# Kernel optimization log

Measured on AMD Instinct MI355X. Metric: run time of the kernel, lower is better.

The kernel has to match this reference:

```python
import jax, jax.numpy as jnp
import numpy as np

IN_CH = 64
INTER = IN_CH // 2
B, H, W = 2, 80, 80


def setup_inputs() -> dict:
    key = jax.random.key(0)
    k = jax.random.split(key, 5)
    s = 1.0 / np.sqrt(IN_CH)
    return {
        "x": jax.random.normal(k[0], (B, IN_CH, H, W), dtype=jnp.float32),
        "g_w": jax.random.normal(k[1], (INTER, IN_CH), dtype=jnp.float32) * s,
        "theta_w": jax.random.normal(k[2], (INTER, IN_CH), dtype=jnp.float32) * s,
        "phi_w": jax.random.normal(k[3], (INTER, IN_CH), dtype=jnp.float32) * s,
        "w_w": jax.random.normal(k[4], (IN_CH, INTER), dtype=jnp.float32) * (1.0 / np.sqrt(INTER)),
    }


def reference(x, g_w, theta_w, phi_w, w_w):
    # Non-local block: 1x1 convs (bias=False) are channel matmuls over N=H*W positions.
    Bc, C, Hh, Ww = x.shape
    N = Hh * Ww
    xf = x.reshape(Bc, C, N)                            # [B, C, N]
    g = jnp.einsum('ic,bcn->bni', g_w, xf)              # [B, N, inter]
    theta = jnp.einsum('ic,bcn->bni', theta_w, xf)      # [B, N, inter]
    phi = jnp.einsum('ic,bcn->bin', phi_w, xf)          # [B, inter, N]
    affinity = jax.nn.softmax(jnp.einsum('bni,bim->bnm', theta, phi), axis=-1)  # [B, N, N]
    y = jnp.einsum('bnm,bmi->bni', affinity, g)         # [B, N, inter]
    y = jnp.einsum('ci,bni->bcn', w_w, y).reshape(Bc, C, Hh, Ww)
    return x + y
```

## Files before the change

### kernel.cpp

```cpp
#include <hip/hip_runtime.h>
#include <math.h>

#define BATCH 2
#define CH    64
#define INTER 32
#define NPOS  6400
#define NTILE 50
#define LOG2E 1.44269504088896f
#define SPLIT 10
#define TPB   5

typedef _Float16 f16x8 __attribute__((ext_vector_type(8)));
typedef _Float16 f16x2 __attribute__((ext_vector_type(2)));
typedef _Float16 h4    __attribute__((ext_vector_type(4)));
typedef float    f32x4 __attribute__((ext_vector_type(4)));

static __device__ __forceinline__ f16x2 pkrtz(float a, float b) {
    return __builtin_bit_cast(f16x2, __builtin_amdgcn_cvt_pkrtz(a, b));
}


__global__ __launch_bounds__(256) void nlb_proj_kernel(
    const float* __restrict__ x,
    const float* __restrict__ g_w,
    const float* __restrict__ th_w,
    const float* __restrict__ ph_w,
    _Float16* __restrict__ Qh, _Float16* __restrict__ Kf,
    _Float16* __restrict__ Vf)
{
    const int b  = blockIdx.z;
    const int p  = blockIdx.y;
    const int n0 = blockIdx.x * 64;
    const int t  = threadIdx.x;
    const int w  = __builtin_amdgcn_readfirstlane(t) >> 6;
    const int lane = t & 63;

    const float* wsrc = (p == 0) ? th_w : (p == 1) ? ph_w : g_w;
    const float* xg = x + (size_t)b * CH * NPOS + n0 + lane;

    float xr[64];
    #pragma unroll
    for (int c = 0; c < 64; c++) xr[c] = xg[(size_t)c * NPOS];

    __shared__ float buf[32][65];

    float accs[8];
    #pragma unroll
    for (int rr = 0; rr < 8; rr++) {
        const int row = w * 8 + rr;
        const float* wr = wsrc + row * 64;
        float a0 = 0.f, a1 = 0.f, a2 = 0.f, a3 = 0.f;
        #pragma unroll
        for (int c = 0; c < 16; c++) {
            a0 += wr[c]      * xr[c];
            a1 += wr[c + 16] * xr[c + 16];
            a2 += wr[c + 32] * xr[c + 32];
            a3 += wr[c + 48] * xr[c + 48];
        }
        accs[rr] = (a0 + a1) + (a2 + a3);
    }

    if (p == 2) {
        const int n  = n0 + lane;
        const int T  = n >> 7, kk = n & 127;
        const int g  = kk >> 4, qd = (kk >> 2) & 3, r3 = kk & 3;
        const int kc = g >> 1, j = (g & 1) * 4 + r3;
        const int half = w >> 1, d15base = (w & 1) * 8;
        _Float16* vb = Vf +
            (((((size_t)b * NTILE + T) * 8 + kc * 2 + half) * 64
              + qd * 16 + d15base) * 8 + j);
        #pragma unroll
        for (int rr = 0; rr < 8; rr++)
            vb[(size_t)rr * 8] = (_Float16)accs[rr];
        return;
    }

    #pragma unroll
    for (int rr = 0; rr < 8; rr++) buf[w * 8 + rr][lane] = accs[rr];
    __syncthreads();

    const int pos = t >> 2, ic = t & 3;
    if (p == 0) {
        f16x8 hv;
        #pragma unroll
        for (int j = 0; j < 8; j++)
            hv[j] = (_Float16)(buf[ic * 8 + j][pos] * LOG2E);
        *(f16x8*)(Qh + ((size_t)b * NPOS + n0 + pos) * 32 + ic * 8) = hv;
    } else {
        f16x8 hv;
        #pragma unroll
        for (int j = 0; j < 8; j++)
            hv[j] = (_Float16)buf[ic * 8 + j][pos];
        const int key = n0 + pos, T = key >> 7, kk = key & 127;
        const int g = kk >> 4, m16 = kk & 15;
        ((f16x8*)Kf)[(((size_t)b * NTILE + T) * 8 + g) * 64 + ic * 16 + m16] = hv;
    }
}

__global__ __launch_bounds__(512) void nlb_flash_kernel(
    const _Float16* __restrict__ Qh, const _Float16* __restrict__ Kf,
    const _Float16* __restrict__ Vf,
    _Float16* __restrict__ Opart, float2* __restrict__ ml)
{
    __shared__ f16x8 smem[5120];

    const int b     = blockIdx.z;
    const int split = blockIdx.y;
    const int t     = threadIdx.x;
    const int w     = t >> 6;
    const int lane  = t & 63;
    const int n16   = lane & 15;
    const int quad  = lane >> 4;
    const int q0    = blockIdx.x * 128 + w * 16;

    const f16x8 qa = *(const f16x8*)(Qh + ((size_t)b * NPOS + q0 + n16) * 32 + quad * 8);

    {
        const f16x8* Ks = (const f16x8*)Kf + ((size_t)b * NTILE + split * TPB) * 512;
        const f16x8* Vs = (const f16x8*)Vf + ((size_t)b * NTILE + split * TPB) * 512;
        f16x8 st[5];
        #pragma unroll
        for (int c = 0; c < 5; c++) st[c] = Ks[c * 512 + t];
        #pragma unroll
        for (int c = 0; c < 5; c++) smem[c * 512 + t] = st[c];
        #pragma unroll
        for (int c = 0; c < 5; c++) st[c] = Vs[c * 512 + t];
        #pragma unroll
        for (int c = 0; c < 5; c++) smem[2560 + c * 512 + t] = st[c];
    }
    __syncthreads();

    f32x4 o0 = (f32x4)0.f;
    f32x4 o1 = (f32x4)0.f;
    float runm = -1e30f, lsum = 0.f;

    for (int i = 0; i < TPB; i++) {
        const int kb = i * 512;
        const int vb = 2560 + i * 512;

        f32x4 sc[8];
        #pragma unroll
        for (int g = 0; g < 8; g++) {
            f16x8 kf = smem[kb + g * 64 + lane];
            f32x4 z = (f32x4)0.f;
            sc[g] = __builtin_amdgcn_mfma_f32_16x16x32_f16(kf, qa, z, 0, 0, 0);
        }

        float m = fmaxf(fmaxf(sc[0][0], sc[0][1]), fmaxf(sc[0][2], sc[0][3]));
        #pragma unroll
        for (int g = 1; g < 8; g++) {
            float mg = fmaxf(fmaxf(sc[g][0], sc[g][1]), fmaxf(sc[g][2], sc[g][3]));
            m = fmaxf(m, mg);
        }
        m = fmaxf(m, __shfl_xor(m, 16));
        m = fmaxf(m, __shfl_xor(m, 32));
        float nm = fmaxf(runm, m);
        float a  = __builtin_amdgcn_exp2f(runm - nm);
        runm = nm;
        float ls = 0.f;
        #pragma unroll
        for (int g = 0; g < 8; g++) {
            #pragma unroll
            for (int r = 0; r < 4; r++) {
                float p = __builtin_amdgcn_exp2f(sc[g][r] - nm);
                sc[g][r] = p;
                ls += p;
            }
        }
        lsum = lsum * a + ls;
        o0 *= a;
        o1 *= a;

        #pragma unroll
        for (int kc = 0; kc < 4; kc++) {
            union { f16x8 v; f16x2 h2[4]; } pb;
            pb.h2[0] = pkrtz(sc[kc * 2][0],     sc[kc * 2][1]);
            pb.h2[1] = pkrtz(sc[kc * 2][2],     sc[kc * 2][3]);
            pb.h2[2] = pkrtz(sc[kc * 2 + 1][0], sc[kc * 2 + 1][1]);
            pb.h2[3] = pkrtz(sc[kc * 2 + 1][2], sc[kc * 2 + 1][3]);
            f16x8 v0 = smem[vb + (kc * 2) * 64 + lane];
            f16x8 v1 = smem[vb + (kc * 2 + 1) * 64 + lane];
            o0 = __builtin_amdgcn_mfma_f32_16x16x32_f16(v0, pb.v, o0, 0, 0, 0);
            o1 = __builtin_amdgcn_mfma_f32_16x16x32_f16(v1, pb.v, o1, 0, 0, 0);
        }
    }

    lsum += __shfl_xor(lsum, 16);
    lsum += __shfl_xor(lsum, 32);
    float invl = 1.f / lsum;
    const size_t base = ((size_t)(b * SPLIT + split) * NPOS + q0 + n16) * 32;
    h4 h0, h1;
    #pragma unroll
    for (int r = 0; r < 4; r++) {
        h0[r] = (_Float16)(o0[r] * invl);
        h1[r] = (_Float16)(o1[r] * invl);
    }
    *(h4*)(Opart + base + quad * 4)      = h0;
    *(h4*)(Opart + base + 16 + quad * 4) = h1;
    if (quad == 0)
        ml[(size_t)(b * SPLIT + split) * NPOS + q0 + n16] = make_float2(runm, lsum);
}

__global__ __launch_bounds__(256) void nlb_combine_kernel(
    const _Float16* __restrict__ Opart, const float2* __restrict__ ml,
    const float* __restrict__ w_w, const float* __restrict__ x,
    float* __restrict__ out)
{
    __shared__ float wf[64][33];
    __shared__ float wts[32][12];
    __shared__ float of[32][33];

    const int b  = blockIdx.y;
    const int q0 = blockIdx.x * 32;
    const int t  = threadIdx.x;

    for (int idx = t; idx < 2048; idx += 256) wf[idx >> 5][idx & 31] = w_w[idx];

    if (t < 32) {
        float2 v[SPLIT];
        float m = -1e30f;
        #pragma unroll
        for (int s = 0; s < SPLIT; s++) {
            v[s] = ml[(size_t)(b * SPLIT + s) * NPOS + q0 + t];
            m = fmaxf(m, v[s].x);
        }
        float suml = 0.f;
        #pragma unroll
        for (int s = 0; s < SPLIT; s++) {
            float wgt = __builtin_amdgcn_exp2f(v[s].x - m) * v[s].y;
            wts[t][s] = wgt;
            suml += wgt;
        }
        float inv = 1.f / suml;
        #pragma unroll
        for (int s = 0; s < SPLIT; s++) wts[t][s] *= inv;
    }
    __syncthreads();

    {
        const int q = t >> 3, dg = t & 7;
        float a0 = 0.f, a1 = 0.f, a2 = 0.f, a3 = 0.f;
        #pragma unroll
        for (int s = 0; s < SPLIT; s++) {
            h4 hv = *(const h4*)(Opart +
                ((size_t)(b * SPLIT + s) * NPOS + q0 + q) * 32 + dg * 4);
            float c = wts[q][s];
            a0 += c * (float)hv[0]; a1 += c * (float)hv[1];
            a2 += c * (float)hv[2]; a3 += c * (float)hv[3];
        }
        of[q][dg * 4]     = a0; of[q][dg * 4 + 1] = a1;
        of[q][dg * 4 + 2] = a2; of[q][dg * 4 + 3] = a3;
    }
    __syncthreads();

    {
        const int q = t & 31, cg = t >> 5;
        const float* xb = x   + (size_t)b * CH * NPOS + q0 + q;
        float*       ob = out + (size_t)b * CH * NPOS + q0 + q;
        #pragma unroll
        for (int cc = 0; cc < 8; cc++) {
            int ch = cg * 8 + cc;
            float acc = 0.f;
            #pragma unroll
            for (int i = 0; i < 32; i++) acc += wf[ch][i] * of[q][i];
            ob[(size_t)ch * NPOS] = acc + xb[(size_t)ch * NPOS];
        }
    }
}

extern "C" void kernel_launch(void* const* d_in, const int* in_sizes, int n_in,
                              void* d_out, int out_size, void* d_ws, size_t ws_size,
                              hipStream_t stream) {
    const float* x    = (const float*)d_in[0];
    const float* g_w  = (const float*)d_in[1];
    const float* th_w = (const float*)d_in[2];
    const float* ph_w = (const float*)d_in[3];
    const float* w_w  = (const float*)d_in[4];
    float* out = (float*)d_out;

    const size_t SZ = (size_t)BATCH * NPOS * INTER;
    _Float16* Qh = (_Float16*)d_ws;
    _Float16* Kf = Qh + SZ;
    _Float16* Vf = Kf + SZ;
    _Float16* Opart = Vf + SZ;
    float2*   ml    = (float2*)(Opart + SZ * SPLIT);

    nlb_proj_kernel<<<dim3(NPOS / 64, 3, BATCH), 256, 0, stream>>>(
        x, g_w, th_w, ph_w, Qh, Kf, Vf);
    nlb_flash_kernel<<<dim3(NPOS / 128, SPLIT, BATCH), 512, 0, stream>>>(
        Qh, Kf, Vf, Opart, ml);
    nlb_combine_kernel<<<dim3(NPOS / 32, BATCH), 256, 0, stream>>>(
        Opart, ml, w_w, x, out);
}
```

Before: 102.5 us.

## Compute all three projections per block and prefetch V fragments in flash loop

The projection kernel now computes the g, theta and phi projections in one block, so each block loads its 64 channels of x into registers once instead of three separate blocks each loading them. The grid shrinks to one third and extra syncthreads guard reuse of the shared buffer. The flash kernel adds a launch-bounds occupancy hint and loads all eight V fragments from LDS before the softmax, so LDS latency can overlap with the exp and max work. The cost is higher register pressure and fewer, longer-running projection blocks.

```diff
diff --git a/kernel.cpp b/kernel.cpp
--- a/kernel.cpp
+++ b/kernel.cpp
@@ -28,14 +28,12 @@
     _Float16* __restrict__ Qh, _Float16* __restrict__ Kf,
     _Float16* __restrict__ Vf)
 {
-    const int b  = blockIdx.z;
-    const int p  = blockIdx.y;
+    const int b  = blockIdx.y;
     const int n0 = blockIdx.x * 64;
     const int t  = threadIdx.x;
     const int w  = __builtin_amdgcn_readfirstlane(t) >> 6;
     const int lane = t & 63;
 
-    const float* wsrc = (p == 0) ? th_w : (p == 1) ? ph_w : g_w;
     const float* xg = x + (size_t)b * CH * NPOS + n0 + lane;
 
     float xr[64];
@@ -43,24 +41,26 @@
     for (int c = 0; c < 64; c++) xr[c] = xg[(size_t)c * NPOS];
 
     __shared__ float buf[32][65];
-
     float accs[8];
-    #pragma unroll
-    for (int rr = 0; rr < 8; rr++) {
-        const int row = w * 8 + rr;
-        const float* wr = wsrc + row * 64;
-        float a0 = 0.f, a1 = 0.f, a2 = 0.f, a3 = 0.f;
-        #pragma unroll
-        for (int c = 0; c < 16; c++) {
-            a0 += wr[c]      * xr[c];
-            a1 += wr[c + 16] * xr[c + 16];
-            a2 += wr[c + 32] * xr[c + 32];
-            a3 += wr[c + 48] * xr[c + 48];
-        }
-        accs[rr] = (a0 + a1) + (a2 + a3);
-    }
-
-    if (p == 2) {
+
+    auto dot8 = [&](const float* __restrict__ wsrc) {
+        #pragma unroll
+        for (int rr = 0; rr < 8; rr++) {
+            const float* wr = wsrc + (w * 8 + rr) * 64;
+            float a0 = 0.f, a1 = 0.f, a2 = 0.f, a3 = 0.f;
+            #pragma unroll
+            for (int c = 0; c < 16; c++) {
+                a0 += wr[c]      * xr[c];
+                a1 += wr[c + 16] * xr[c + 16];
+                a2 += wr[c + 32] * xr[c + 32];
+                a3 += wr[c + 48] * xr[c + 48];
+            }
+            accs[rr] = (a0 + a1) + (a2 + a3);
+        }
+    };
+
+    dot8(g_w);
+    {
         const int n  = n0 + lane;
         const int T  = n >> 7, kk = n & 127;
         const int g  = kk >> 4, qd = (kk >> 2) & 3, r3 = kk & 3;
@@ -72,21 +72,28 @@
         #pragma unroll
         for (int rr = 0; rr < 8; rr++)
             vb[(size_t)rr * 8] = (_Float16)accs[rr];
-        return;
-    }
-
+    }
+
+    const int pos = t >> 2, ic = t & 3;
+
+    dot8(th_w);
     #pragma unroll
     for (int rr = 0; rr < 8; rr++) buf[w * 8 + rr][lane] = accs[rr];
     __syncthreads();
-
-    const int pos = t >> 2, ic = t & 3;
-    if (p == 0) {
+    {
         f16x8 hv;
         #pragma unroll
         for (int j = 0; j < 8; j++)
             hv[j] = (_Float16)(buf[ic * 8 + j][pos] * LOG2E);
         *(f16x8*)(Qh + ((size_t)b * NPOS + n0 + pos) * 32 + ic * 8) = hv;
-    } else {
+    }
+    __syncthreads();
+
+    dot8(ph_w);
+    #pragma unroll
+    for (int rr = 0; rr < 8; rr++) buf[w * 8 + rr][lane] = accs[rr];
+    __syncthreads();
+    {
         f16x8 hv;
         #pragma unroll
         for (int j = 0; j < 8; j++)
@@ -97,7 +104,7 @@
     }
 }
 
-__global__ __launch_bounds__(512) void nlb_flash_kernel(
+__global__ __launch_bounds__(512, 4) void nlb_flash_kernel(
     const _Float16* __restrict__ Qh, const _Float16* __restrict__ Kf,
     const _Float16* __restrict__ Vf,
     _Float16* __restrict__ Opart, float2* __restrict__ ml)
@@ -146,12 +153,16 @@
             sc[g] = __builtin_amdgcn_mfma_f32_16x16x32_f16(kf, qa, z, 0, 0, 0);
         }
 
-        float m = fmaxf(fmaxf(sc[0][0], sc[0][1]), fmaxf(sc[0][2], sc[0][3]));
-        #pragma unroll
-        for (int g = 1; g < 8; g++) {
-            float mg = fmaxf(fmaxf(sc[g][0], sc[g][1]), fmaxf(sc[g][2], sc[g][3]));
-            m = fmaxf(m, mg);
-        }
+        f16x8 vr[8];
+        #pragma unroll
+        for (int u = 0; u < 8; u++) vr[u] = smem[vb + u * 64 + lane];
+
+        float mg[8];
+        #pragma unroll
+        for (int g = 0; g < 8; g++)
+            mg[g] = fmaxf(fmaxf(sc[g][0], sc[g][1]), fmaxf(sc[g][2], sc[g][3]));
+        float m = fmaxf(fmaxf(fmaxf(mg[0], mg[1]), fmaxf(mg[2], mg[3])),
+                        fmaxf(fmaxf(mg[4], mg[5]), fmaxf(mg[6], mg[7])));
         m = fmaxf(m, __shfl_xor(m, 16));
         m = fmaxf(m, __shfl_xor(m, 32));
         float nm = fmaxf(runm, m);
@@ -178,10 +189,8 @@
             pb.h2[1] = pkrtz(sc[kc * 2][2],     sc[kc * 2][3]);
             pb.h2[2] = pkrtz(sc[kc * 2 + 1][0], sc[kc * 2 + 1][1]);
             pb.h2[3] = pkrtz(sc[kc * 2 + 1][2], sc[kc * 2 + 1][3]);
-            f16x8 v0 = smem[vb + (kc * 2) * 64 + lane];
-            f16x8 v1 = smem[vb + (kc * 2 + 1) * 64 + lane];
-            o0 = __builtin_amdgcn_mfma_f32_16x16x32_f16(v0, pb.v, o0, 0, 0, 0);
-            o1 = __builtin_amdgcn_mfma_f32_16x16x32_f16(v1, pb.v, o1, 0, 0, 0);
+            o0 = __builtin_amdgcn_mfma_f32_16x16x32_f16(vr[kc * 2],     pb.v, o0, 0, 0, 0);
+            o1 = __builtin_amdgcn_mfma_f32_16x16x32_f16(vr[kc * 2 + 1], pb.v, o1, 0, 0, 0);
         }
     }
 
@@ -285,7 +294,7 @@
     _Float16* Opart = Vf + SZ;
     float2*   ml    = (float2*)(Opart + SZ * SPLIT);
 
-    nlb_proj_kernel<<<dim3(NPOS / 64, 3, BATCH), 256, 0, stream>>>(
+    nlb_proj_kernel<<<dim3(NPOS / 64, BATCH), 256, 0, stream>>>(
         x, g_w, th_w, ph_w, Qh, Kf, Vf);
     nlb_flash_kernel<<<dim3(NPOS / 128, SPLIT, BATCH), 512, 0, stream>>>(
         Qh, Kf, Vf, Opart, ml);
```

Measured after the change: 107.2 us. +4.6%, slower.

## Process two query tiles per wave in flash kernel, halving block size

Applied to the files above, without the earlier changes.

Each wave of the flash-attention kernel now handles 32 query rows (two 16-row tiles) instead of 16, so every K/V fragment read from shared memory feeds two MFMAs. Blocks shrink from 512 to 256 threads while keeping 128 queries per block, and the staging loop loads twice as many chunks per thread. This cuts LDS traffic per unit of work and adds independent MFMA chains for latency hiding, at the cost of higher register pressure and fewer waves per block.

```diff
diff --git a/kernel.cpp b/kernel.cpp
--- a/kernel.cpp
+++ b/kernel.cpp
@@ -97,7 +97,7 @@
     }
 }
 
-__global__ __launch_bounds__(512) void nlb_flash_kernel(
+__global__ __launch_bounds__(256, 2) void nlb_flash_kernel(
     const _Float16* __restrict__ Qh, const _Float16* __restrict__ Kf,
     const _Float16* __restrict__ Vf,
     _Float16* __restrict__ Opart, float2* __restrict__ ml)
@@ -111,94 +111,140 @@
     const int lane  = t & 63;
     const int n16   = lane & 15;
     const int quad  = lane >> 4;
-    const int q0    = blockIdx.x * 128 + w * 16;
-
-    const f16x8 qa = *(const f16x8*)(Qh + ((size_t)b * NPOS + q0 + n16) * 32 + quad * 8);
+    const int q0    = blockIdx.x * 128 + w * 32;
+
+    const f16x8 qa0 = *(const f16x8*)(Qh + ((size_t)b * NPOS + q0 + n16) * 32 + quad * 8);
+    const f16x8 qa1 = *(const f16x8*)(Qh + ((size_t)b * NPOS + q0 + 16 + n16) * 32 + quad * 8);
 
     {
         const f16x8* Ks = (const f16x8*)Kf + ((size_t)b * NTILE + split * TPB) * 512;
         const f16x8* Vs = (const f16x8*)Vf + ((size_t)b * NTILE + split * TPB) * 512;
-        f16x8 st[5];
-        #pragma unroll
-        for (int c = 0; c < 5; c++) st[c] = Ks[c * 512 + t];
-        #pragma unroll
-        for (int c = 0; c < 5; c++) smem[c * 512 + t] = st[c];
-        #pragma unroll
-        for (int c = 0; c < 5; c++) st[c] = Vs[c * 512 + t];
-        #pragma unroll
-        for (int c = 0; c < 5; c++) smem[2560 + c * 512 + t] = st[c];
+        f16x8 st[10];
+        #pragma unroll
+        for (int c = 0; c < 10; c++) st[c] = Ks[c * 256 + t];
+        #pragma unroll
+        for (int c = 0; c < 10; c++) smem[c * 256 + t] = st[c];
+        #pragma unroll
+        for (int c = 0; c < 10; c++) st[c] = Vs[c * 256 + t];
+        #pragma unroll
+        for (int c = 0; c < 10; c++) smem[2560 + c * 256 + t] = st[c];
     }
     __syncthreads();
 
-    f32x4 o0 = (f32x4)0.f;
-    f32x4 o1 = (f32x4)0.f;
-    float runm = -1e30f, lsum = 0.f;
+    f32x4 o00 = (f32x4)0.f, o01 = (f32x4)0.f;
+    f32x4 o10 = (f32x4)0.f, o11 = (f32x4)0.f;
+    float runm0 = -1e30f, lsum0 = 0.f;
+    float runm1 = -1e30f, lsum1 = 0.f;
 
     for (int i = 0; i < TPB; i++) {
         const int kb = i * 512;
         const int vb = 2560 + i * 512;
 
-        f32x4 sc[8];
+        f32x4 sc0[8], sc1[8];
         #pragma unroll
         for (int g = 0; g < 8; g++) {
             f16x8 kf = smem[kb + g * 64 + lane];
             f32x4 z = (f32x4)0.f;
-            sc[g] = __builtin_amdgcn_mfma_f32_16x16x32_f16(kf, qa, z, 0, 0, 0);
-        }
-
-        float m = fmaxf(fmaxf(sc[0][0], sc[0][1]), fmaxf(sc[0][2], sc[0][3]));
-        #pragma unroll
-        for (int g = 1; g < 8; g++) {
-            float mg = fmaxf(fmaxf(sc[g][0], sc[g][1]), fmaxf(sc[g][2], sc[g][3]));
-            m = fmaxf(m, mg);
-        }
-        m = fmaxf(m, __shfl_xor(m, 16));
-        m = fmaxf(m, __shfl_xor(m, 32));
-        float nm = fmaxf(runm, m);
-        float a  = __builtin_amdgcn_exp2f(runm - nm);
-        runm = nm;
-        float ls = 0.f;
-        #pragma unroll
-        for (int g = 0; g < 8; g++) {
-            #pragma unroll
-            for (int r = 0; r < 4; r++) {
-                float p = __builtin_amdgcn_exp2f(sc[g][r] - nm);
-                sc[g][r] = p;
-                ls += p;
+            sc0[g] = __builtin_amdgcn_mfma_f32_16x16x32_f16(kf, qa0, z, 0, 0, 0);
+            sc1[g] = __builtin_amdgcn_mfma_f32_16x16x32_f16(kf, qa1, z, 0, 0, 0);
+        }
+
+        {
+            float mg[8];
+            #pragma unroll
+            for (int g = 0; g < 8; g++)
+                mg[g] = fmaxf(fmaxf(sc0[g][0], sc0[g][1]), fmaxf(sc0[g][2], sc0[g][3]));
+            float m = fmaxf(fmaxf(fmaxf(mg[0], mg[1]), fmaxf(mg[2], mg[3])),
+                            fmaxf(fmaxf(mg[4], mg[5]), fmaxf(mg[6], mg[7])));
+            m = fmaxf(m, __shfl_xor(m, 16));
+            m = fmaxf(m, __shfl_xor(m, 32));
+            float nm = fmaxf(runm0, m);
+            float a  = __builtin_amdgcn_exp2f(runm0 - nm);
+            runm0 = nm;
+            float ls = 0.f;
+            #pragma unroll
+            for (int g = 0; g < 8; g++) {
+                #pragma unroll
+                for (int r = 0; r < 4; r++) {
+                    float p = __builtin_amdgcn_exp2f(sc0[g][r] - nm);
+                    sc0[g][r] = p;
+                    ls += p;
+                }
             }
-        }
-        lsum = lsum * a + ls;
-        o0 *= a;
-        o1 *= a;
+            lsum0 = lsum0 * a + ls;
+            o00 *= a;
+            o01 *= a;
+        }
+        {
+            float mg[8];
+            #pragma unroll
+            for (int g = 0; g < 8; g++)
+                mg[g] = fmaxf(fmaxf(sc1[g][0], sc1[g][1]), fmaxf(sc1[g][2], sc1[g][3]));
+            float m = fmaxf(fmaxf(fmaxf(mg[0], mg[1]), fmaxf(mg[2], mg[3])),
+                            fmaxf(fmaxf(mg[4], mg[5]), fmaxf(mg[6], mg[7])));
+            m = fmaxf(m, __shfl_xor(m, 16));
+            m = fmaxf(m, __shfl_xor(m, 32));
+            float nm = fmaxf(runm1, m);
+            float a  = __builtin_amdgcn_exp2f(runm1 - nm);
+            runm1 = nm;
+            float ls = 0.f;
+            #pragma unroll
+            for (int g = 0; g < 8; g++) {
+                #pragma unroll
+                for (int r = 0; r < 4; r++) {
+                    float p = __builtin_amdgcn_exp2f(sc1[g][r] - nm);
+                    sc1[g][r] = p;
+                    ls += p;
+                }
+            }
+            lsum1 = lsum1 * a + ls;
+            o10 *= a;
+            o11 *= a;
+        }
 
         #pragma unroll
         for (int kc = 0; kc < 4; kc++) {
-            union { f16x8 v; f16x2 h2[4]; } pb;
-            pb.h2[0] = pkrtz(sc[kc * 2][0],     sc[kc * 2][1]);
-            pb.h2[1] = pkrtz(sc[kc * 2][2],     sc[kc * 2][3]);
-            pb.h2[2] = pkrtz(sc[kc * 2 + 1][0], sc[kc * 2 + 1][1]);
-            pb.h2[3] = pkrtz(sc[kc * 2 + 1][2], sc[kc * 2 + 1][3]);
+            union { f16x8 v; f16x2 h2[4]; } pb0, pb1;
+            pb0.h2[0] = pkrtz(sc0[kc * 2][0],     sc0[kc * 2][1]);
+            pb0.h2[1] = pkrtz(sc0[kc * 2][2],     sc0[kc * 2][3]);
+            pb0.h2[2] = pkrtz(sc0[kc * 2 + 1][0], sc0[kc * 2 + 1][1]);
+            pb0.h2[3] = pkrtz(sc0[kc * 2 + 1][2], sc0[kc * 2 + 1][3]);
+            pb1.h2[0] = pkrtz(sc1[kc * 2][0],     sc1[kc * 2][1]);
+            pb1.h2[1] = pkrtz(sc1[kc * 2][2],     sc1[kc * 2][3]);
+            pb1.h2[2] = pkrtz(sc1[kc * 2 + 1][0], sc1[kc * 2 + 1][1]);
+            pb1.h2[3] = pkrtz(sc1[kc * 2 + 1][2], sc1[kc * 2 + 1][3]);
             f16x8 v0 = smem[vb + (kc * 2) * 64 + lane];
             f16x8 v1 = smem[vb + (kc * 2 + 1) * 64 + lane];
-            o0 = __builtin_amdgcn_mfma_f32_16x16x32_f16(v0, pb.v, o0, 0, 0, 0);
-            o1 = __builtin_amdgcn_mfma_f32_16x16x32_f16(v1, pb.v, o1, 0, 0, 0);
-        }
-    }
-
-    lsum += __shfl_xor(lsum, 16);
-    lsum += __shfl_xor(lsum, 32);
-    float invl = 1.f / lsum;
-    const size_t base = ((size_t)(b * SPLIT + split) * NPOS + q0 + n16) * 32;
-    h4 h0, h1;
+            o00 = __builtin_amdgcn_mfma_f32_16x16x32_f16(v0, pb0.v, o00, 0, 0, 0);
+            o01 = __builtin_amdgcn_mfma_f32_16x16x32_f16(v1, pb0.v, o01, 0, 0, 0);
+            o10 = __builtin_amdgcn_mfma_f32_16x16x32_f16(v0, pb1.v, o10, 0, 0, 0);
+            o11 = __builtin_amdgcn_mfma_f32_16x16x32_f16(v1, pb1.v, o11, 0, 0, 0);
+        }
+    }
+
+    lsum0 += __shfl_xor(lsum0, 16);
+    lsum0 += __shfl_xor(lsum0, 32);
+    lsum1 += __shfl_xor(lsum1, 16);
+    lsum1 += __shfl_xor(lsum1, 32);
+    const float inv0 = 1.f / lsum0, inv1 = 1.f / lsum1;
+    const size_t base0 = ((size_t)(b * SPLIT + split) * NPOS + q0 + n16) * 32;
+    const size_t base1 = base0 + (size_t)16 * 32;
+    h4 h00, h01, h10, h11;
     #pragma unroll
     for (int r = 0; r < 4; r++) {
-        h0[r] = (_Float16)(o0[r] * invl);
-        h1[r] = (_Float16)(o1[r] * invl);
-    }
-    *(h4*)(Opart + base + quad * 4)      = h0;
-    *(h4*)(Opart + base + 16 + quad * 4) = h1;
-    if (quad == 0)
-        ml[(size_t)(b * SPLIT + split) * NPOS + q0 + n16] = make_float2(runm, lsum);
+        h00[r] = (_Float16)(o00[r] * inv0);
+        h01[r] = (_Float16)(o01[r] * inv0);
+        h10[r] = (_Float16)(o10[r] * inv1);
+        h11[r] = (_Float16)(o11[r] * inv1);
+    }
+    *(h4*)(Opart + base0 + quad * 4)      = h00;
+    *(h4*)(Opart + base0 + 16 + quad * 4) = h01;
+    *(h4*)(Opart + base1 + quad * 4)      = h10;
+    *(h4*)(Opart + base1 + 16 + quad * 4) = h11;
+    if (quad == 0) {
+        ml[(size_t)(b * SPLIT + split) * NPOS + q0 + n16]      = make_float2(runm0, lsum0);
+        ml[(size_t)(b * SPLIT + split) * NPOS + q0 + 16 + n16] = make_float2(runm1, lsum1);
+    }
 }
 
 __global__ __launch_bounds__(256) void nlb_combine_kernel(
@@ -287,7 +333,7 @@
 
     nlb_proj_kernel<<<dim3(NPOS / 64, 3, BATCH), 256, 0, stream>>>(
         x, g_w, th_w, ph_w, Qh, Kf, Vf);
-    nlb_flash_kernel<<<dim3(NPOS / 128, SPLIT, BATCH), 512, 0, stream>>>(
+    nlb_flash_kernel<<<dim3(NPOS / 128, SPLIT, BATCH), 256, 0, stream>>>(
         Qh, Kf, Vf, Opart, ml);
     nlb_combine_kernel<<<dim3(NPOS / 32, BATCH), 256, 0, stream>>>(
         Opart, ml, w_w, x, out);
```

Measured after the change: 104.5 us. No clear change (+1.9%).

## Stream K/V tiles from global into registers instead of staging in LDS

Applied to the files above, without the earlier changes.

The flash kernel no longer copies its K/V split into shared memory behind a block barrier. Each wave now loads its K and V fragments directly from global (L2-cached) memory into registers and prefetches the next K tile while computing softmax. Blocks shrink from 512 to 256 threads so more blocks fit per CU, with launch bounds asking for 4 blocks. This removes LDS usage and the barrier, but each wave re-reads K/V from cache and register pressure goes up.

```diff
diff --git a/kernel.cpp b/kernel.cpp
--- a/kernel.cpp
+++ b/kernel.cpp
@@ -97,13 +97,11 @@
     }
 }
 
-__global__ __launch_bounds__(512) void nlb_flash_kernel(
+__global__ __launch_bounds__(256, 4) void nlb_flash_kernel(
     const _Float16* __restrict__ Qh, const _Float16* __restrict__ Kf,
     const _Float16* __restrict__ Vf,
     _Float16* __restrict__ Opart, float2* __restrict__ ml)
 {
-    __shared__ f16x8 smem[5120];
-
     const int b     = blockIdx.z;
     const int split = blockIdx.y;
     const int t     = threadIdx.x;
@@ -111,47 +109,46 @@
     const int lane  = t & 63;
     const int n16   = lane & 15;
     const int quad  = lane >> 4;
-    const int q0    = blockIdx.x * 128 + w * 16;
+    const int q0    = blockIdx.x * 64 + w * 16;
 
     const f16x8 qa = *(const f16x8*)(Qh + ((size_t)b * NPOS + q0 + n16) * 32 + quad * 8);
 
-    {
-        const f16x8* Ks = (const f16x8*)Kf + ((size_t)b * NTILE + split * TPB) * 512;
-        const f16x8* Vs = (const f16x8*)Vf + ((size_t)b * NTILE + split * TPB) * 512;
-        f16x8 st[5];
-        #pragma unroll
-        for (int c = 0; c < 5; c++) st[c] = Ks[c * 512 + t];
-        #pragma unroll
-        for (int c = 0; c < 5; c++) smem[c * 512 + t] = st[c];
-        #pragma unroll
-        for (int c = 0; c < 5; c++) st[c] = Vs[c * 512 + t];
-        #pragma unroll
-        for (int c = 0; c < 5; c++) smem[2560 + c * 512 + t] = st[c];
-    }
-    __syncthreads();
+    const f16x8* __restrict__ Ku =
+        (const f16x8*)Kf + ((size_t)b * NTILE + split * TPB) * 512 + lane;
+    const f16x8* __restrict__ Vu =
+        (const f16x8*)Vf + ((size_t)b * NTILE + split * TPB) * 512 + lane;
 
     f32x4 o0 = (f32x4)0.f;
     f32x4 o1 = (f32x4)0.f;
     float runm = -1e30f, lsum = 0.f;
 
+    f16x8 kr[8], vr[8];
+    #pragma unroll
+    for (int g = 0; g < 8; g++) kr[g] = Ku[g * 64];
+
+    #pragma unroll
     for (int i = 0; i < TPB; i++) {
-        const int kb = i * 512;
-        const int vb = 2560 + i * 512;
-
         f32x4 sc[8];
         #pragma unroll
         for (int g = 0; g < 8; g++) {
-            f16x8 kf = smem[kb + g * 64 + lane];
             f32x4 z = (f32x4)0.f;
-            sc[g] = __builtin_amdgcn_mfma_f32_16x16x32_f16(kf, qa, z, 0, 0, 0);
-        }
-
-        float m = fmaxf(fmaxf(sc[0][0], sc[0][1]), fmaxf(sc[0][2], sc[0][3]));
-        #pragma unroll
-        for (int g = 1; g < 8; g++) {
-            float mg = fmaxf(fmaxf(sc[g][0], sc[g][1]), fmaxf(sc[g][2], sc[g][3]));
-            m = fmaxf(m, mg);
-        }
+            sc[g] = __builtin_amdgcn_mfma_f32_16x16x32_f16(kr[g], qa, z, 0, 0, 0);
+        }
+
+        #pragma unroll
+        for (int u = 0; u < 8; u++) vr[u] = Vu[i * 512 + u * 64];
+
+        if (i + 1 < TPB) {
+            #pragma unroll
+            for (int g = 0; g < 8; g++) kr[g] = Ku[(i + 1) * 512 + g * 64];
+        }
+
+        float mg[8];
+        #pragma unroll
+        for (int g = 0; g < 8; g++)
+            mg[g] = fmaxf(fmaxf(sc[g][0], sc[g][1]), fmaxf(sc[g][2], sc[g][3]));
+        float m = fmaxf(fmaxf(fmaxf(mg[0], mg[1]), fmaxf(mg[2], mg[3])),
+                        fmaxf(fmaxf(mg[4], mg[5]), fmaxf(mg[6], mg[7])));
         m = fmaxf(m, __shfl_xor(m, 16));
         m = fmaxf(m, __shfl_xor(m, 32));
         float nm = fmaxf(runm, m);
@@ -178,10 +175,8 @@
             pb.h2[1] = pkrtz(sc[kc * 2][2],     sc[kc * 2][3]);
             pb.h2[2] = pkrtz(sc[kc * 2 + 1][0], sc[kc * 2 + 1][1]);
             pb.h2[3] = pkrtz(sc[kc * 2 + 1][2], sc[kc * 2 + 1][3]);
-            f16x8 v0 = smem[vb + (kc * 2) * 64 + lane];
-            f16x8 v1 = smem[vb + (kc * 2 + 1) * 64 + lane];
-            o0 = __builtin_amdgcn_mfma_f32_16x16x32_f16(v0, pb.v, o0, 0, 0, 0);
-            o1 = __builtin_amdgcn_mfma_f32_16x16x32_f16(v1, pb.v, o1, 0, 0, 0);
+            o0 = __builtin_amdgcn_mfma_f32_16x16x32_f16(vr[kc * 2],     pb.v, o0, 0, 0, 0);
+            o1 = __builtin_amdgcn_mfma_f32_16x16x32_f16(vr[kc * 2 + 1], pb.v, o1, 0, 0, 0);
         }
     }
 
@@ -287,7 +282,7 @@
 
     nlb_proj_kernel<<<dim3(NPOS / 64, 3, BATCH), 256, 0, stream>>>(
         x, g_w, th_w, ph_w, Qh, Kf, Vf);
-    nlb_flash_kernel<<<dim3(NPOS / 128, SPLIT, BATCH), 512, 0, stream>>>(
+    nlb_flash_kernel<<<dim3(NPOS / 64, SPLIT, BATCH), 256, 0, stream>>>(
         Qh, Kf, Vf, Opart, ml);
     nlb_combine_kernel<<<dim3(NPOS / 32, BATCH), 256, 0, stream>>>(
         Opart, ml, w_w, x, out);
```

Result: slower. 161.8 us (+57.8%).
